# Performance work log

Hardware: AMD Instinct MI355X
Metric: run time of the kernel (lower is better)

The kernel has to match this reference:

```python
import jax, jax.numpy as jnp
import numpy as np

# Sizes (match input_specs)
B = 50                 # number of CRN graphs in the batch
NS_PER, NR_PER = 2000, 4000
N_S, N_R = B * NS_PER, B * NR_PER   # 100k species, 200k reactions total
E = 1_000_000          # bipartite edges
D = 128                # d_model
L = 2                  # n_layers
N_TYPES, P_DIM = 16, 8
MAX_SPECIES_IDX = 2000


def setup_inputs() -> dict:
    key = jax.random.key(0)
    ks = jax.random.split(key, 12)
    inp = {
        "species_indices": jax.random.randint(ks[0], (N_S,), 0, MAX_SPECIES_IDX, dtype=jnp.int32),
        "is_external": jax.random.randint(ks[1], (N_S,), 0, 2, dtype=jnp.int32),
        "propensity_type_ids": jax.random.randint(ks[2], (N_R,), 0, N_TYPES, dtype=jnp.int32),
        "propensity_params": jax.random.normal(ks[3], (N_R, P_DIM), dtype=jnp.float32),
        "edge_species": jax.random.randint(ks[4], (E,), 0, N_S, dtype=jnp.int32),
        "edge_reaction": jax.random.randint(ks[5], (E,), 0, N_R, dtype=jnp.int32),
        # contiguous per-graph segment ids (graphs are equal-sized)
        "species_batch": jnp.repeat(jnp.arange(B, dtype=jnp.int32), NS_PER),
        "reaction_batch": jnp.repeat(jnp.arange(B, dtype=jnp.int32), NR_PER),
        # learned parameters
        "species_table": jax.random.normal(ks[6], (MAX_SPECIES_IDX, D), dtype=jnp.float32) * 0.02,
        "external_table": jax.random.normal(ks[7], (2, D), dtype=jnp.float32) * 0.02,
        "type_table": jax.random.normal(ks[8], (N_TYPES, D), dtype=jnp.float32) * 0.02,
        "W_param": jax.random.normal(ks[9], (P_DIM, D), dtype=jnp.float32) * 0.1,
        "b_param": jnp.zeros((D,), dtype=jnp.float32),
        # per-layer message-passing weights: concat([h, msg]) -> d
        "Wr": jax.random.normal(ks[10], (L, 2 * D, D), dtype=jnp.float32) * 0.05,
        "br": jnp.zeros((L, D), dtype=jnp.float32),
        "Ws": jax.random.normal(ks[11], (L, 2 * D, D), dtype=jnp.float32) * 0.05,
        "bs": jnp.zeros((L, D), dtype=jnp.float32),
    }
    return inp


def reference(species_indices, is_external, propensity_type_ids, propensity_params,
              edge_species, edge_reaction, species_batch, reaction_batch,
              species_table, external_table, type_table, W_param, b_param,
              Wr, br, Ws, bs):
    # Initial embeddings
    h_s = species_table[species_indices] + external_table[is_external]          # (N_S, D)
    h_r = type_table[propensity_type_ids] + propensity_params @ W_param + b_param  # (N_R, D)

    n_s, n_r = h_s.shape[0], h_r.shape[0]
    # Alternating bipartite sum message passing (SumMessagePassingLayer)
    for l in range(Wr.shape[0]):
        m_r = jax.ops.segment_sum(h_s[edge_species], edge_reaction, num_segments=n_r)
        h_r = jax.nn.relu(jnp.concatenate([h_r, m_r], axis=-1) @ Wr[l] + br[l])
        m_s = jax.ops.segment_sum(h_r[edge_reaction], edge_species, num_segments=n_s)
        h_s = jax.nn.relu(jnp.concatenate([h_s, m_s], axis=-1) @ Ws[l] + bs[l])

    # Segment-mean pooling per graph (index_add then divide by counts)
    pooled_s = jax.ops.segment_sum(h_s, species_batch, num_segments=B) / float(NS_PER)
    pooled_r = jax.ops.segment_sum(h_r, reaction_batch, num_segments=B) / float(NR_PER)
    context = jnp.concatenate([pooled_s, pooled_r], axis=-1)  # (B, 2D); dropout p=0 -> identity
    return context
```

## Files before the change

kernel.cpp:

```cpp
#include <hip/hip_runtime.h>
#include <stdint.h>

#define NS 100000
#define NR 200000
#define EE 1000000
#define DD 128
#define NB 50
#define NSP 2000
#define NRP 4000
#define BSH 10
#define NBR 196
#define NBS 98
#define CHUNK 8192

typedef short bf16x8 __attribute__((ext_vector_type(8)));
typedef float f32x4 __attribute__((ext_vector_type(4)));
typedef unsigned u32x4 __attribute__((ext_vector_type(4)));
typedef unsigned u32x2 __attribute__((ext_vector_type(2)));

__device__ __forceinline__ unsigned short f2bf(float f){
  unsigned u = __float_as_uint(f);
  u = (u + 0x7FFFu + ((u >> 16) & 1u)) >> 16;
  return (unsigned short)u;
}
__device__ __forceinline__ float bf2f(unsigned short s){
  return __uint_as_float(((unsigned)s) << 16);
}
__device__ __forceinline__ unsigned packbf(float a, float b){
  return (unsigned)f2bf(a) | ((unsigned)f2bf(b) << 16);
}
__device__ __forceinline__ float bflo(unsigned p){ return __uint_as_float(p << 16); }
__device__ __forceinline__ float bfhi(unsigned p){ return __uint_as_float(p & 0xFFFF0000u); }

__global__ void pack_w(const float* __restrict__ Wr, const float* __restrict__ Ws,
                       unsigned short* __restrict__ Wp){
  int g = blockIdx.x*256 + threadIdx.x;
  if (g >= 4*32768) return;
  int j = g & 7; int rest = g >> 3;
  int lane = rest & 63; rest >>= 6;
  int ks = rest & 7; rest >>= 3;
  int ct = rest & 7; int mat = rest >> 3;
  int k  = ks*32 + (lane >> 4)*8 + j;
  int cc = ct*16 + (lane & 15);
  const float* src = (mat < 2) ? (Wr + (size_t)mat*256*DD) : (Ws + (size_t)(mat-2)*256*DD);
  Wp[g] = f2bf(src[(size_t)k*DD + cc]);
}

__global__ __launch_bounds__(256) void init_all(const int* __restrict__ si, const int* __restrict__ ext,
        const int* __restrict__ tid, const float* __restrict__ pp,
        const float* __restrict__ st, const float* __restrict__ et, const float* __restrict__ tt,
        const float* __restrict__ Wpar, const float* __restrict__ bpar,
        unsigned short* __restrict__ hs, unsigned short* __restrict__ hr){
  int g = blockIdx.x*256 + threadIdx.x;
  int row = g >> 4, colb = (g & 15) * 8;
  if (row < NS){
    const float* a = st + (size_t)si[row]*DD + colb;
    const float* b = et + (size_t)ext[row]*DD + colb;
    float4 x0 = ((const float4*)a)[0], x1 = ((const float4*)a)[1];
    float4 y0 = ((const float4*)b)[0], y1 = ((const float4*)b)[1];
    u32x4 o;
    o.x = packbf(x0.x+y0.x, x0.y+y0.y);
    o.y = packbf(x0.z+y0.z, x0.w+y0.w);
    o.z = packbf(x1.x+y1.x, x1.y+y1.y);
    o.w = packbf(x1.z+y1.z, x1.w+y1.w);
    *(u32x4*)(hs + (size_t)row*DD + colb) = o;
  } else {
    int r = row - NS;
    const float* tb = tt + (size_t)tid[r]*DD + colb;
    float4 a0 = ((const float4*)tb)[0], a1 = ((const float4*)tb)[1];
    float4 b0 = ((const float4*)(bpar+colb))[0], b1 = ((const float4*)(bpar+colb))[1];
    a0.x += b0.x; a0.y += b0.y; a0.z += b0.z; a0.w += b0.w;
    a1.x += b1.x; a1.y += b1.y; a1.z += b1.z; a1.w += b1.w;
    const float* pr = pp + (size_t)r*8;
    float4 p0 = ((const float4*)pr)[0], p1 = ((const float4*)pr)[1];
    float w[8] = {p0.x,p0.y,p0.z,p0.w,p1.x,p1.y,p1.z,p1.w};
    #pragma unroll
    for (int p = 0; p < 8; p++){
      float4 w0 = ((const float4*)(Wpar + p*DD + colb))[0];
      float4 w1 = ((const float4*)(Wpar + p*DD + colb))[1];
      a0.x += w[p]*w0.x; a0.y += w[p]*w0.y; a0.z += w[p]*w0.z; a0.w += w[p]*w0.w;
      a1.x += w[p]*w1.x; a1.y += w[p]*w1.y; a1.z += w[p]*w1.z; a1.w += w[p]*w1.w;
    }
    u32x4 o;
    o.x = packbf(a0.x, a0.y); o.y = packbf(a0.z, a0.w);
    o.z = packbf(a1.x, a1.y); o.w = packbf(a1.z, a1.w);
    *(u32x4*)(hr + (size_t)r*DD + colb) = o;
  }
}

__global__ __launch_bounds__(256) void bucket_hist(const int* __restrict__ er, const int* __restrict__ es,
                                                   int* __restrict__ gcnt){
  __shared__ int cnt[NBR + NBS];
  int t = threadIdx.x;
  for (int j = t; j < NBR + NBS; j += 256) cnt[j] = 0;
  __syncthreads();
  long i0 = (long)blockIdx.x * 2048;
  for (int j = t; j < 2048; j += 256){
    long i = i0 + j;
    if (i < EE){
      atomicAdd(&cnt[er[i] >> BSH], 1);
      atomicAdd(&cnt[NBR + (es[i] >> BSH)], 1);
    }
  }
  __syncthreads();
  for (int j = t; j < NBR + NBS; j += 256)
    if (cnt[j]) atomicAdd(&gcnt[j], cnt[j]);
}

__global__ __launch_bounds__(256) void bucket_scan(const int* __restrict__ gcnt,
        int* __restrict__ bktOffR, int* __restrict__ bktOffS,
        int* __restrict__ gCurR, int* __restrict__ gCurS){
  __shared__ int a[256];
  int t = threadIdx.x;
  int own = (t < NBR) ? gcnt[t] : 0;
  a[t] = own; __syncthreads();
  for (int d = 1; d < 256; d <<= 1){
    int x = (t >= d) ? a[t-d] : 0;
    __syncthreads(); a[t] += x; __syncthreads();
  }
  if (t < NBR){ int v = a[t] - own; bktOffR[t] = v; gCurR[t] = v; }
  if (t == 0) bktOffR[NBR] = EE;
  __syncthreads();
  own = (t < NBS) ? gcnt[NBR + t] : 0;
  a[t] = own; __syncthreads();
  for (int d = 1; d < 256; d <<= 1){
    int x = (t >= d) ? a[t-d] : 0;
    __syncthreads(); a[t] += x; __syncthreads();
  }
  if (t < NBS){ int v = a[t] - own; bktOffS[t] = v; gCurS[t] = v; }
  if (t == 0) bktOffS[NBS] = EE;
}

__global__ __launch_bounds__(256) void bin_edges(const int* __restrict__ er, const int* __restrict__ es,
        int* __restrict__ gCurR, int* __restrict__ gCurS,
        unsigned* __restrict__ recR, unsigned* __restrict__ recS){
  __shared__ unsigned stage[CHUNK];
  __shared__ unsigned char stageb[CHUNK];
  __shared__ int cnt[256], scn[256], pref[256], gbase[256], lcur[256];
  int t = threadIdx.x;
  int side = blockIdx.y;
  const int* dest = side ? es : er;
  const int* srca = side ? er : es;
  int* gCur = side ? gCurS : gCurR;
  unsigned* rec = side ? recS : recR;
  int nbkt = side ? NBS : NBR;
  long i0 = (long)blockIdx.x * CHUNK;
  int n = (EE - i0 < CHUNK) ? (int)(EE - i0) : CHUNK;
  cnt[t] = 0;
  __syncthreads();
  for (int j = t; j < n; j += 256)
    atomicAdd(&cnt[dest[i0 + j] >> BSH], 1);
  __syncthreads();
  scn[t] = cnt[t];
  __syncthreads();
  for (int d = 1; d < 256; d <<= 1){
    int x = (t >= d) ? scn[t-d] : 0;
    __syncthreads(); scn[t] += x; __syncthreads();
  }
  pref[t] = scn[t] - cnt[t];
  lcur[t] = scn[t] - cnt[t];
  if (t < nbkt && cnt[t] > 0) gbase[t] = atomicAdd(&gCur[t], cnt[t]);
  __syncthreads();
  for (int j = t; j < n; j += 256){
    int d = dest[i0 + j];
    int s = srca[i0 + j];
    int b = d >> BSH;
    int p = atomicAdd(&lcur[b], 1);
    stage[p] = ((unsigned)(d - (b << BSH)) << 18) | (unsigned)s;
    stageb[p] = (unsigned char)b;
  }
  __syncthreads();
  for (int e = t; e < n; e += 256){
    int b = stageb[e];
    rec[gbase[b] + (e - pref[b])] = stage[e];
  }
}

__global__ __launch_bounds__(256) void build_csr(const unsigned* __restrict__ recR, const unsigned* __restrict__ recS,
        const int* __restrict__ bktOffR, const int* __restrict__ bktOffS,
        unsigned* __restrict__ csrR, unsigned* __restrict__ csrS,
        int* __restrict__ offsR, int* __restrict__ offsS){
  __shared__ int hist[1024], pref[1024], cur[1024], ws[256];
  int t = threadIdx.x;
  int bb = blockIdx.x;
  const unsigned* rec; const int* bktOff; unsigned* csr; int* offs; int N;
  if (bb < NBR){ rec = recR; bktOff = bktOffR; csr = csrR; offs = offsR; N = NR; }
  else { bb -= NBR; rec = recS; bktOff = bktOffS; csr = csrS; offs = offsS; N = NS; }
  int d0 = bb << BSH;
  int base = bktOff[bb], cnt_ = bktOff[bb+1] - base;
  #pragma unroll
  for (int j = 0; j < 4; j++) hist[t*4+j] = 0;
  __syncthreads();
  for (int e = t; e < cnt_; e += 256)
    atomicAdd(&hist[rec[base + e] >> 18], 1);
  __syncthreads();
  int s = 0, h[4];
  #pragma unroll
  for (int j = 0; j < 4; j++){ h[j] = hist[t*4+j]; s += h[j]; }
  ws[t] = s;
  __syncthreads();
  for (int d = 1; d < 256; d <<= 1){
    int x = (t >= d) ? ws[t-d] : 0;
    __syncthreads(); ws[t] += x; __syncthreads();
  }
  int run = ws[t] - s;
  #pragma unroll
  for (int j = 0; j < 4; j++){ pref[t*4+j] = run; cur[t*4+j] = base + run; run += h[j]; }
  __syncthreads();
  int DPB = N - d0; if (DPB > 1024) DPB = 1024;
  #pragma unroll
  for (int j = 0; j < 4; j++){
    int i = t*4 + j;
    if (i < DPB) offs[d0 + i] = base + pref[i];
  }
  if (t == 0 && d0 + DPB == N) offs[N] = EE;
  __syncthreads();
  for (int e = t; e < cnt_; e += 256){
    unsigned r = rec[base + e];
    int pos = atomicAdd(&cur[r >> 18], 1);
    csr[pos] = (((r >> 18) & 31u) << 26) | ((r & 0x3FFFFu) << 8);
  }
}

__global__ __launch_bounds__(256) void fused_layer(
        const unsigned short* __restrict__ gsrc,
        const unsigned short* __restrict__ hself,
        const int* __restrict__ offs, const unsigned* __restrict__ csr,
        const unsigned short* __restrict__ Wp, const float* __restrict__ bias,
        unsigned short* __restrict__ hout)
{
  __shared__ unsigned short msgT[32*DD];
  int t = threadIdx.x;
  int lane = t & 63;
  int w = t >> 6;
  int quad = lane >> 4, rlo = lane & 15;
  int row0 = blockIdx.x * 32;

  for (int i = t; i < 2048; i += 256) ((unsigned*)msgT)[i] = 0u;
  __syncthreads();

  {
    int rbeg = row0 + w*8;
    int k  = __builtin_amdgcn_readfirstlane(offs[rbeg]);
    int ke = __builtin_amdgcn_readfirstlane(offs[rbeg + 8]);
    int c16 = lane >> 2, sub4 = lane & 3;
    const char* gbase = (const char*)gsrc;
    float a0 = 0.f, a1 = 0.f;
    int cur = -1;
    unsigned rc[8]; unsigned pv[8];
    if (k < ke){
      #pragma unroll
      for (int i = 0; i < 8; i++){
        int kk = (k + i < ke) ? (k + i) : (ke - 1);
        rc[i] = (unsigned)__builtin_amdgcn_readfirstlane(csr[kk]);
      }
      #pragma unroll
      for (int i = 0; i < 8; i++)
        pv[i] = *(const unsigned*)(gbase + (rc[i] & 0x03FFFF00u) + lane*4);
      while (k < ke){
        unsigned rc2[8], pv2[8];
        int kn = k + 8;
        #pragma unroll
        for (int i = 0; i < 8; i++){
          int kk = (kn + i < ke) ? (kn + i) : (ke - 1);
          rc2[i] = (unsigned)__builtin_amdgcn_readfirstlane(csr[kk]);
        }
        #pragma unroll
        for (int i = 0; i < 8; i++)
          pv2[i] = *(const unsigned*)(gbase + (rc2[i] & 0x03FFFF00u) + lane*4);
        #pragma unroll
        for (int i = 0; i < 8; i++){
          if (k + i < ke){
            int dl = (int)(rc[i] >> 26);
            if (dl != cur){
              if (cur >= 0)
                *(unsigned*)(msgT + cur*DD + ((c16 ^ (cur & 7)) << 3) + (sub4 << 1)) = packbf(a0, a1);
              a0 = 0.f; a1 = 0.f;
              cur = dl;
            }
            a0 += bflo(pv[i]); a1 += bfhi(pv[i]);
          }
        }
        #pragma unroll
        for (int i = 0; i < 8; i++){ rc[i] = rc2[i]; pv[i] = pv2[i]; }
        k = kn;
      }
      if (cur >= 0)
        *(unsigned*)(msgT + cur*DD + ((c16 ^ (cur & 7)) << 3) + (sub4 << 1)) = packbf(a0, a1);
    }
  }
  __syncthreads();

  int ct0 = w * 2;
  bf16x8 wf[16];
  #pragma unroll
  for (int ks = 0; ks < 8; ks++){
    wf[ks*2+0] = *(const bf16x8*)(Wp + (size_t)(((ct0+0)*8 + ks)*64 + lane) * 8);
    wf[ks*2+1] = *(const bf16x8*)(Wp + (size_t)(((ct0+1)*8 + ks)*64 + lane) * 8);
  }
  bf16x8 Hb0[4], Hb1[4];
  #pragma unroll
  for (int ks = 0; ks < 4; ks++){
    int kloc = ks*32 + quad*8;
    Hb0[ks] = *(const bf16x8*)(hself + (size_t)(row0 + rlo) * DD + kloc);
    Hb1[ks] = *(const bf16x8*)(hself + (size_t)(row0 + 16 + rlo) * DD + kloc);
  }
  bf16x8 Mb0[4], Mb1[4];
  #pragma unroll
  for (int ks2 = 0; ks2 < 4; ks2++){
    int c8 = ks2*4 + quad;
    int lr0 = rlo, lr1 = 16 + rlo;
    Mb0[ks2] = *(const bf16x8*)(msgT + lr0*DD + ((c8 ^ (lr0 & 7)) * 8));
    Mb1[ks2] = *(const bf16x8*)(msgT + lr1*DD + ((c8 ^ (lr1 & 7)) * 8));
  }

  f32x4 acc[2][2];
  #pragma unroll
  for (int i = 0; i < 2; i++)
    #pragma unroll
    for (int j = 0; j < 2; j++){ f32x4 z = {0.f,0.f,0.f,0.f}; acc[i][j] = z; }

  #pragma unroll
  for (int ks = 0; ks < 4; ks++){
    acc[0][0] = __builtin_amdgcn_mfma_f32_16x16x32_bf16(wf[ks*2+0], Hb0[ks], acc[0][0], 0, 0, 0);
    acc[0][1] = __builtin_amdgcn_mfma_f32_16x16x32_bf16(wf[ks*2+1], Hb0[ks], acc[0][1], 0, 0, 0);
    acc[1][0] = __builtin_amdgcn_mfma_f32_16x16x32_bf16(wf[ks*2+0], Hb1[ks], acc[1][0], 0, 0, 0);
    acc[1][1] = __builtin_amdgcn_mfma_f32_16x16x32_bf16(wf[ks*2+1], Hb1[ks], acc[1][1], 0, 0, 0);
  }
  #pragma unroll
  for (int ks2 = 0; ks2 < 4; ks2++){
    int ks = 4 + ks2;
    acc[0][0] = __builtin_amdgcn_mfma_f32_16x16x32_bf16(wf[ks*2+0], Mb0[ks2], acc[0][0], 0, 0, 0);
    acc[0][1] = __builtin_amdgcn_mfma_f32_16x16x32_bf16(wf[ks*2+1], Mb0[ks2], acc[0][1], 0, 0, 0);
    acc[1][0] = __builtin_amdgcn_mfma_f32_16x16x32_bf16(wf[ks*2+0], Mb1[ks2], acc[1][0], 0, 0, 0);
    acc[1][1] = __builtin_amdgcn_mfma_f32_16x16x32_bf16(wf[ks*2+1], Mb1[ks2], acc[1][1], 0, 0, 0);
  }

  #pragma unroll
  for (int c = 0; c < 2; c++){
    float4 bv = *(const float4*)(bias + (ct0+c)*16 + quad*4);
    #pragma unroll
    for (int rb = 0; rb < 2; rb++){
      int row = row0 + rb*16 + rlo;
      float v0 = acc[rb][c][0] + bv.x;
      float v1 = acc[rb][c][1] + bv.y;
      float v2 = acc[rb][c][2] + bv.z;
      float v3 = acc[rb][c][3] + bv.w;
      v0 = v0 > 0.f ? v0 : 0.f;
      v1 = v1 > 0.f ? v1 : 0.f;
      v2 = v2 > 0.f ? v2 : 0.f;
      v3 = v3 > 0.f ? v3 : 0.f;
      u32x2 o; o.x = packbf(v0, v1); o.y = packbf(v2, v3);
      *(u32x2*)(hout + (size_t)row*DD + (ct0+c)*16 + quad*4) = o;
    }
  }
}

__global__ __launch_bounds__(256) void pool(const unsigned short* __restrict__ hs,
        const unsigned short* __restrict__ hr, float* __restrict__ out){
  __shared__ float red[16][128];
  int b = blockIdx.x, part = blockIdx.y;
  int t = threadIdx.x;
  int rg = t >> 4, sub = t & 15;
  const unsigned short* src; int row0, outoff; float scale;
  if (part < 4){ src = hs; row0 = b*NSP + part*500; outoff = b*256; scale = 1.f/NSP; }
  else { src = hr; row0 = b*NRP + (part-4)*500; outoff = b*256 + 128; scale = 1.f/NRP; }
  float a0=0,a1=0,a2=0,a3=0,a4=0,a5=0,a6=0,a7=0;
  for (int r = rg; r < 500; r += 16){
    u32x4 p = *(const u32x4*)(src + (size_t)(row0+r)*DD + sub*8);
    a0 += bflo(p.x); a1 += bfhi(p.x);
    a2 += bflo(p.y); a3 += bfhi(p.y);
    a4 += bflo(p.z); a5 += bfhi(p.z);
    a6 += bflo(p.w); a7 += bfhi(p.w);
  }
  float* rr = &red[rg][sub*8];
  rr[0]=a0; rr[1]=a1; rr[2]=a2; rr[3]=a3; rr[4]=a4; rr[5]=a5; rr[6]=a6; rr[7]=a7;
  __syncthreads();
  if (t < 128){
    float s = 0.f;
    #pragma unroll
    for (int g = 0; g < 16; g++) s += red[g][t];
    atomicAdd(&out[outoff + t], s * scale);
  }
}

extern "C" void kernel_launch(void* const* d_in, const int* in_sizes, int n_in,
                              void* d_out, int out_size, void* d_ws, size_t ws_size,
                              hipStream_t stream)
{
  const int*   si   = (const int*)d_in[0];
  const int*   ext  = (const int*)d_in[1];
  const int*   tid  = (const int*)d_in[2];
  const float* pp   = (const float*)d_in[3];
  const int*   es   = (const int*)d_in[4];
  const int*   er   = (const int*)d_in[5];
  const float* st   = (const float*)d_in[8];
  const float* et   = (const float*)d_in[9];
  const float* tt   = (const float*)d_in[10];
  const float* Wpar = (const float*)d_in[11];
  const float* bpar = (const float*)d_in[12];
  const float* Wr   = (const float*)d_in[13];
  const float* br   = (const float*)d_in[14];
  const float* Ws   = (const float*)d_in[15];
  const float* bs   = (const float*)d_in[16];
  float* out = (float*)d_out;

  char* basep = (char*)d_ws; size_t off = 0;
  auto alloc = [&](size_t bytes)->char*{
    char* r = basep + off; off = (off + bytes + 255) & ~(size_t)255; return r;
  };
  unsigned short* hs0 = (unsigned short*)alloc((size_t)NS*DD*2);
  unsigned short* hs1 = (unsigned short*)alloc((size_t)NS*DD*2);
  unsigned short* hr0 = (unsigned short*)alloc((size_t)NR*DD*2);
  unsigned short* hr1 = (unsigned short*)alloc((size_t)NR*DD*2);
  unsigned short* Wp  = (unsigned short*)alloc((size_t)4*32768*2);
  int* offsR = (int*)alloc((size_t)(NR+1)*4);
  int* offsS = (int*)alloc((size_t)(NS+1)*4);
  unsigned* csrR = (unsigned*)alloc((size_t)EE*4);
  unsigned* csrS = (unsigned*)alloc((size_t)EE*4);
  int* gcnt   = (int*)alloc(2048);
  int* bktOffR= (int*)alloc(2048);
  int* bktOffS= (int*)alloc(2048);
  int* gCurR  = (int*)alloc(2048);
  int* gCurS  = (int*)alloc(2048);
  unsigned* recR = (unsigned*)hs1;
  unsigned* recS = (unsigned*)hr1;

  hipMemsetAsync(gcnt, 0, 2048, stream);
  hipMemsetAsync(d_out, 0, (size_t)out_size*4, stream);

  pack_w<<<512, 256, 0, stream>>>(Wr, Ws, Wp);
  init_all<<<(NS+NR)*16/256, 256, 0, stream>>>(si, ext, tid, pp, st, et, tt, Wpar, bpar, hs0, hr0);

  bucket_hist<<<(EE + 2047)/2048, 256, 0, stream>>>(er, es, gcnt);
  bucket_scan<<<1, 256, 0, stream>>>(gcnt, bktOffR, bktOffS, gCurR, gCurS);
  bin_edges<<<dim3((EE + CHUNK - 1)/CHUNK, 2), 256, 0, stream>>>(er, es, gCurR, gCurS, recR, recS);
  build_csr<<<NBR + NBS, 256, 0, stream>>>(recR, recS, bktOffR, bktOffS, csrR, csrS, offsR, offsS);

  fused_layer<<<NR/32, 256, 0, stream>>>(hs0, hr0, offsR, csrR, Wp + (size_t)0*32768, br + (size_t)0*DD, hr1);
  fused_layer<<<NS/32, 256, 0, stream>>>(hr1, hs0, offsS, csrS, Wp + (size_t)2*32768, bs + (size_t)0*DD, hs1);
  fused_layer<<<NR/32, 256, 0, stream>>>(hs1, hr1, offsR, csrR, Wp + (size_t)1*32768, br + (size_t)1*DD, hr0);
  fused_layer<<<NS/32, 256, 0, stream>>>(hr0, hs1, offsS, csrS, Wp + (size_t)3*32768, bs + (size_t)1*DD, hs0);

  pool<<<dim3(NB, 12), 256, 0, stream>>>(hs0, hr0, out);
}
```

Baseline: 461.4 us.

## Split each wave into two half-waves gathering alternate edges with padded CSR

Each destination's edge list is padded to an even length, with a dummy edge pointing at an appended zero row. Each wavefront then splits into two 32-lane halves that gather even and odd edges at the same time, each lane loading 8 bytes instead of 4. Partial sums go into two separate LDS message buffers that are added in bf16 before the MFMA stage. This doubles edges in flight per wave and widens loads to hide gather latency. The cost is padding work, twice the LDS, an extra bf16 rounding step and a separate ends array.

```diff
diff --git a/kernel.cpp b/kernel.cpp
--- a/kernel.cpp
+++ b/kernel.cpp
@@ -12,6 +12,7 @@
 #define NBR 196
 #define NBS 98
 #define CHUNK 8192
+#define RING 8
 
 typedef short bf16x8 __attribute__((ext_vector_type(8)));
 typedef float f32x4 __attribute__((ext_vector_type(4)));
@@ -31,6 +32,16 @@
 }
 __device__ __forceinline__ float bflo(unsigned p){ return __uint_as_float(p << 16); }
 __device__ __forceinline__ float bfhi(unsigned p){ return __uint_as_float(p & 0xFFFF0000u); }
+
+__device__ __forceinline__ bf16x8 addbf8(bf16x8 a, bf16x8 b){
+  union { bf16x8 v; u32x4 u; } A, B, R;
+  A.v = a; B.v = b;
+  R.u.x = packbf(bflo(A.u.x)+bflo(B.u.x), bfhi(A.u.x)+bfhi(B.u.x));
+  R.u.y = packbf(bflo(A.u.y)+bflo(B.u.y), bfhi(A.u.y)+bfhi(B.u.y));
+  R.u.z = packbf(bflo(A.u.z)+bflo(B.u.z), bfhi(A.u.z)+bfhi(B.u.z));
+  R.u.w = packbf(bflo(A.u.w)+bflo(B.u.w), bfhi(A.u.w)+bfhi(B.u.w));
+  return R.v;
+}
 
 __global__ void pack_w(const float* __restrict__ Wr, const float* __restrict__ Ws,
                        unsigned short* __restrict__ Wp){
@@ -179,24 +190,26 @@
 __global__ __launch_bounds__(256) void build_csr(const unsigned* __restrict__ recR, const unsigned* __restrict__ recS,
         const int* __restrict__ bktOffR, const int* __restrict__ bktOffS,
         unsigned* __restrict__ csrR, unsigned* __restrict__ csrS,
-        int* __restrict__ offsR, int* __restrict__ offsS){
+        int* __restrict__ offsR, int* __restrict__ offsS,
+        int* __restrict__ endsR, int* __restrict__ endsS){
   __shared__ int hist[1024], pref[1024], cur[1024], ws[256];
   int t = threadIdx.x;
   int bb = blockIdx.x;
-  const unsigned* rec; const int* bktOff; unsigned* csr; int* offs; int N;
-  if (bb < NBR){ rec = recR; bktOff = bktOffR; csr = csrR; offs = offsR; N = NR; }
-  else { bb -= NBR; rec = recS; bktOff = bktOffS; csr = csrS; offs = offsS; N = NS; }
+  const unsigned* rec; const int* bktOff; unsigned* csr; int* offs; int* ends; int N; int padsrc;
+  if (bb < NBR){ rec = recR; bktOff = bktOffR; csr = csrR; offs = offsR; ends = endsR; N = NR; padsrc = NS; }
+  else { bb -= NBR; rec = recS; bktOff = bktOffS; csr = csrS; offs = offsS; ends = endsS; N = NS; padsrc = NR; }
   int d0 = bb << BSH;
   int base = bktOff[bb], cnt_ = bktOff[bb+1] - base;
+  int basePad = base + (bb << 10);
   #pragma unroll
   for (int j = 0; j < 4; j++) hist[t*4+j] = 0;
   __syncthreads();
   for (int e = t; e < cnt_; e += 256)
     atomicAdd(&hist[rec[base + e] >> 18], 1);
   __syncthreads();
-  int s = 0, h[4];
-  #pragma unroll
-  for (int j = 0; j < 4; j++){ h[j] = hist[t*4+j]; s += h[j]; }
+  int s = 0, h[4], hp[4];
+  #pragma unroll
+  for (int j = 0; j < 4; j++){ h[j] = hist[t*4+j]; hp[j] = h[j] + (h[j] & 1); s += hp[j]; }
   ws[t] = s;
   __syncthreads();
   for (int d = 1; d < 256; d <<= 1){
@@ -205,15 +218,21 @@
   }
   int run = ws[t] - s;
   #pragma unroll
-  for (int j = 0; j < 4; j++){ pref[t*4+j] = run; cur[t*4+j] = base + run; run += h[j]; }
+  for (int j = 0; j < 4; j++){ pref[t*4+j] = run; cur[t*4+j] = basePad + run; run += hp[j]; }
   __syncthreads();
   int DPB = N - d0; if (DPB > 1024) DPB = 1024;
   #pragma unroll
   for (int j = 0; j < 4; j++){
     int i = t*4 + j;
-    if (i < DPB) offs[d0 + i] = base + pref[i];
-  }
-  if (t == 0 && d0 + DPB == N) offs[N] = EE;
+    if (i < DPB){
+      int hb = hist[i];
+      int hpd = hb + (hb & 1);
+      offs[d0 + i] = basePad + pref[i];
+      ends[d0 + i] = basePad + pref[i] + hpd;
+      if (hb & 1)
+        csr[basePad + pref[i] + hb] = ((unsigned)(i & 31u) << 26) | ((unsigned)padsrc << 8);
+    }
+  }
   __syncthreads();
   for (int e = t; e < cnt_; e += 256){
     unsigned r = rec[base + e];
@@ -225,68 +244,81 @@
 __global__ __launch_bounds__(256) void fused_layer(
         const unsigned short* __restrict__ gsrc,
         const unsigned short* __restrict__ hself,
-        const int* __restrict__ offs, const unsigned* __restrict__ csr,
+        const int* __restrict__ offs, const int* __restrict__ ends,
+        const unsigned* __restrict__ csr,
         const unsigned short* __restrict__ Wp, const float* __restrict__ bias,
         unsigned short* __restrict__ hout)
 {
-  __shared__ unsigned short msgT[32*DD];
+  __shared__ unsigned short msgT2[2*32*DD];
   int t = threadIdx.x;
   int lane = t & 63;
   int w = t >> 6;
   int quad = lane >> 4, rlo = lane & 15;
   int row0 = blockIdx.x * 32;
 
-  for (int i = t; i < 2048; i += 256) ((unsigned*)msgT)[i] = 0u;
+  for (int i = t; i < 4096; i += 256) ((unsigned*)msgT2)[i] = 0u;
   __syncthreads();
 
   {
     int rbeg = row0 + w*8;
     int k  = __builtin_amdgcn_readfirstlane(offs[rbeg]);
-    int ke = __builtin_amdgcn_readfirstlane(offs[rbeg + 8]);
-    int c16 = lane >> 2, sub4 = lane & 3;
-    const char* gbase = (const char*)gsrc;
-    float a0 = 0.f, a1 = 0.f;
+    int ke = __builtin_amdgcn_readfirstlane(ends[rbeg + 7]);
+    int half = lane >> 5, h = lane & 31;
+    int hoff = h * 8;
+    int hbase = half * 4096 ;
+    int c = h >> 1, sub = h & 1;
+    const char* gb = (const char*)gsrc;
+    float a0=0.f, a1=0.f, a2=0.f, a3=0.f;
     int cur = -1;
-    unsigned rc[8]; unsigned pv[8];
+    unsigned rcE[RING]; u32x2 pv[RING];
     if (k < ke){
       #pragma unroll
-      for (int i = 0; i < 8; i++){
-        int kk = (k + i < ke) ? (k + i) : (ke - 1);
-        rc[i] = (unsigned)__builtin_amdgcn_readfirstlane(csr[kk]);
+      for (int i = 0; i < RING; i++){
+        int kp = (k + 2*i + 1 < ke) ? (k + 2*i) : (ke - 2);
+        unsigned re = (unsigned)__builtin_amdgcn_readfirstlane(csr[kp]);
+        unsigned ro = (unsigned)__builtin_amdgcn_readfirstlane(csr[kp+1]);
+        rcE[i] = re;
+        int ve = (int)(re & 0x03FFFF00u), vo = (int)(ro & 0x03FFFF00u);
+        int off = (half ? vo : ve) + hoff;
+        pv[i] = *(const u32x2*)(gb + off);
       }
-      #pragma unroll
-      for (int i = 0; i < 8; i++)
-        pv[i] = *(const unsigned*)(gbase + (rc[i] & 0x03FFFF00u) + lane*4);
       while (k < ke){
-        unsigned rc2[8], pv2[8];
-        int kn = k + 8;
+        int kn = k + 2*RING;
+        unsigned rcE2[RING]; u32x2 pv2[RING];
         #pragma unroll
-        for (int i = 0; i < 8; i++){
-          int kk = (kn + i < ke) ? (kn + i) : (ke - 1);
-          rc2[i] = (unsigned)__builtin_amdgcn_readfirstlane(csr[kk]);
+        for (int i = 0; i < RING; i++){
+          int kp = (kn + 2*i + 1 < ke) ? (kn + 2*i) : (ke - 2);
+          unsigned re = (unsigned)__builtin_amdgcn_readfirstlane(csr[kp]);
+          unsigned ro = (unsigned)__builtin_amdgcn_readfirstlane(csr[kp+1]);
+          rcE2[i] = re;
+          int ve = (int)(re & 0x03FFFF00u), vo = (int)(ro & 0x03FFFF00u);
+          int off = (half ? vo : ve) + hoff;
+          pv2[i] = *(const u32x2*)(gb + off);
         }
         #pragma unroll
-        for (int i = 0; i < 8; i++)
-          pv2[i] = *(const unsigned*)(gbase + (rc2[i] & 0x03FFFF00u) + lane*4);
-        #pragma unroll
-        for (int i = 0; i < 8; i++){
-          if (k + i < ke){
-            int dl = (int)(rc[i] >> 26);
+        for (int i = 0; i < RING; i++){
+          if (k + 2*i < ke){
+            int dl = (int)(rcE[i] >> 26);
             if (dl != cur){
-              if (cur >= 0)
-                *(unsigned*)(msgT + cur*DD + ((c16 ^ (cur & 7)) << 3) + (sub4 << 1)) = packbf(a0, a1);
-              a0 = 0.f; a1 = 0.f;
+              if (cur >= 0){
+                u32x2 o; o.x = packbf(a0, a1); o.y = packbf(a2, a3);
+                *(u32x2*)(msgT2 + hbase + cur*DD + (((c ^ (cur & 7)) << 3) + (sub << 2))) = o;
+              }
+              a0=0.f; a1=0.f; a2=0.f; a3=0.f;
               cur = dl;
             }
-            a0 += bflo(pv[i]); a1 += bfhi(pv[i]);
+            a0 += bflo(pv[i].x); a1 += bfhi(pv[i].x);
+            a2 += bflo(pv[i].y); a3 += bfhi(pv[i].y);
           }
         }
         #pragma unroll
-        for (int i = 0; i < 8; i++){ rc[i] = rc2[i]; pv[i] = pv2[i]; }
+        for (int i = 0; i < RING; i++){ rcE[i] = rcE2[i]; pv[i] = pv2[i]; }
         k = kn;
       }
-      if (cur >= 0)
-        *(unsigned*)(msgT + cur*DD + ((c16 ^ (cur & 7)) << 3) + (sub4 << 1)) = packbf(a0, a1);
+      if (cur >= 0){
+        u32x2 o; o.x = packbf(a0, a1); o.y = packbf(a2, a3);
+        *(u32x2*)(msgT2 + hbase + cur*DD + (((c ^ (cur & 7)) << 3) + (sub << 2))) = o;
+      }
     }
   }
   __syncthreads();
@@ -310,8 +342,14 @@
   for (int ks2 = 0; ks2 < 4; ks2++){
     int c8 = ks2*4 + quad;
     int lr0 = rlo, lr1 = 16 + rlo;
-    Mb0[ks2] = *(const bf16x8*)(msgT + lr0*DD + ((c8 ^ (lr0 & 7)) * 8));
-    Mb1[ks2] = *(const bf16x8*)(msgT + lr1*DD + ((c8 ^ (lr1 & 7)) * 8));
+    int o0 = lr0*DD + ((c8 ^ (lr0 & 7)) << 3);
+    int o1 = lr1*DD + ((c8 ^ (lr1 & 7)) << 3);
+    bf16x8 A0 = *(const bf16x8*)(msgT2 + o0);
+    bf16x8 B0 = *(const bf16x8*)(msgT2 + 4096 + o0);
+    bf16x8 A1 = *(const bf16x8*)(msgT2 + o1);
+    bf16x8 B1 = *(const bf16x8*)(msgT2 + 4096 + o1);
+    Mb0[ks2] = addbf8(A0, B0);
+    Mb1[ks2] = addbf8(A1, B1);
   }
 
   f32x4 acc[2][2];
@@ -409,15 +447,17 @@
   auto alloc = [&](size_t bytes)->char*{
     char* r = basep + off; off = (off + bytes + 255) & ~(size_t)255; return r;
   };
-  unsigned short* hs0 = (unsigned short*)alloc((size_t)NS*DD*2);
-  unsigned short* hs1 = (unsigned short*)alloc((size_t)NS*DD*2);
-  unsigned short* hr0 = (unsigned short*)alloc((size_t)NR*DD*2);
-  unsigned short* hr1 = (unsigned short*)alloc((size_t)NR*DD*2);
+  unsigned short* hs0 = (unsigned short*)alloc((size_t)(NS+1)*DD*2);
+  unsigned short* hs1 = (unsigned short*)alloc((size_t)(NS+1)*DD*2);
+  unsigned short* hr0 = (unsigned short*)alloc((size_t)(NR+1)*DD*2);
+  unsigned short* hr1 = (unsigned short*)alloc((size_t)(NR+1)*DD*2);
   unsigned short* Wp  = (unsigned short*)alloc((size_t)4*32768*2);
-  int* offsR = (int*)alloc((size_t)(NR+1)*4);
-  int* offsS = (int*)alloc((size_t)(NS+1)*4);
-  unsigned* csrR = (unsigned*)alloc((size_t)EE*4);
-  unsigned* csrS = (unsigned*)alloc((size_t)EE*4);
+  int* offsR = (int*)alloc((size_t)NR*4);
+  int* offsS = (int*)alloc((size_t)NS*4);
+  int* endsR = (int*)alloc((size_t)NR*4);
+  int* endsS = (int*)alloc((size_t)NS*4);
+  unsigned* csrR = (unsigned*)alloc((size_t)(EE + NBR*1024)*4);
+  unsigned* csrS = (unsigned*)alloc((size_t)(EE + NBS*1024)*4);
   int* gcnt   = (int*)alloc(2048);
   int* bktOffR= (int*)alloc(2048);
   int* bktOffS= (int*)alloc(2048);
@@ -428,6 +468,10 @@
 
   hipMemsetAsync(gcnt, 0, 2048, stream);
   hipMemsetAsync(d_out, 0, (size_t)out_size*4, stream);
+  hipMemsetAsync(hs0 + (size_t)NS*DD, 0, DD*2, stream);
+  hipMemsetAsync(hs1 + (size_t)NS*DD, 0, DD*2, stream);
+  hipMemsetAsync(hr0 + (size_t)NR*DD, 0, DD*2, stream);
+  hipMemsetAsync(hr1 + (size_t)NR*DD, 0, DD*2, stream);
 
   pack_w<<<512, 256, 0, stream>>>(Wr, Ws, Wp);
   init_all<<<(NS+NR)*16/256, 256, 0, stream>>>(si, ext, tid, pp, st, et, tt, Wpar, bpar, hs0, hr0);
@@ -435,12 +479,13 @@
   bucket_hist<<<(EE + 2047)/2048, 256, 0, stream>>>(er, es, gcnt);
   bucket_scan<<<1, 256, 0, stream>>>(gcnt, bktOffR, bktOffS, gCurR, gCurS);
   bin_edges<<<dim3((EE + CHUNK - 1)/CHUNK, 2), 256, 0, stream>>>(er, es, gCurR, gCurS, recR, recS);
-  build_csr<<<NBR + NBS, 256, 0, stream>>>(recR, recS, bktOffR, bktOffS, csrR, csrS, offsR, offsS);
-
-  fused_layer<<<NR/32, 256, 0, stream>>>(hs0, hr0, offsR, csrR, Wp + (size_t)0*32768, br + (size_t)0*DD, hr1);
-  fused_layer<<<NS/32, 256, 0, stream>>>(hr1, hs0, offsS, csrS, Wp + (size_t)2*32768, bs + (size_t)0*DD, hs1);
-  fused_layer<<<NR/32, 256, 0, stream>>>(hs1, hr1, offsR, csrR, Wp + (size_t)1*32768, br + (size_t)1*DD, hr0);
-  fused_layer<<<NS/32, 256, 0, stream>>>(hr0, hs1, offsS, csrS, Wp + (size_t)3*32768, bs + (size_t)1*DD, hs0);
+  build_csr<<<NBR + NBS, 256, 0, stream>>>(recR, recS, bktOffR, bktOffS, csrR, csrS,
+                                           offsR, offsS, endsR, endsS);
+
+  fused_layer<<<NR/32, 256, 0, stream>>>(hs0, hr0, offsR, endsR, csrR, Wp + (size_t)0*32768, br + (size_t)0*DD, hr1);
+  fused_layer<<<NS/32, 256, 0, stream>>>(hr1, hs0, offsS, endsS, csrS, Wp + (size_t)2*32768, bs + (size_t)0*DD, hs1);
+  fused_layer<<<NR/32, 256, 0, stream>>>(hs1, hr1, offsR, endsR, csrR, Wp + (size_t)1*32768, br + (size_t)1*DD, hr0);
+  fused_layer<<<NS/32, 256, 0, stream>>>(hr0, hs1, offsS, endsS, csrS, Wp + (size_t)3*32768, bs + (size_t)1*DD, hs0);
 
   pool<<<dim3(NB, 12), 256, 0, stream>>>(hs0, hr0, out);
 }
```

Result: slower. 515.3 us (+11.7%).
